# Performance work log

Measured on AMD Instinct MI355X. Metric: run time of the kernel, lower is better.

Reference implementation:

```python
import jax, jax.numpy as jnp
import numpy as np

N, T = 8, 64
V = [2048, 1024, 512, 256, 128]
E = [12288, 6144, 3072, 1536, 768]
NF = [1, 8, 16, 32, 64, 128]
LAT, INIT_DIM = 64, 16
K3 = 27  # 3x3x3 spline kernel bank


def setup_inputs():
    ks = iter(jax.random.split(jax.random.key(0), 80))
    inp = {}
    inp['x'] = jax.random.normal(next(ks), (N, V[0], T), jnp.float32)
    for l in range(5):
        inp['edge_index%d' % l] = jax.random.randint(next(ks), (2, E[l]), 0, V[l])
        inp['edge_attr%d' % l] = jax.random.uniform(next(ks), (E[l], 3), jnp.float32)
    pools = {'P01': (V[1], V[0]), 'P12': (V[2], V[1]), 'P23': (V[3], V[2]), 'P34': (V[4], V[3]),
             'P43': (V[3], V[4]), 'P32': (V[2], V[3]), 'P21': (V[1], V[2]), 'P10': (V[0], V[1])}
    for n, sh in pools.items():
        inp[n] = jax.random.normal(next(ks), sh, jnp.float32) / np.float32(np.sqrt(sh[1]))
    convs = {'conv1_w': (NF[0], NF[1]), 'conv2_w': (NF[1], NF[2]), 'conv3_w': (NF[2], NF[3]), 'conv4_w': (NF[3], NF[4]),
             'deconv4_w': (NF[4], NF[3]), 'deconv3_w': (NF[3], NF[2]), 'deconv2_w': (NF[2], NF[1]), 'deconv1_w': (NF[1], NF[0])}
    for n, (ci, co) in convs.items():
        inp[n] = jax.random.normal(next(ks), (K3, ci, co), jnp.float32) / np.float32(np.sqrt(ci * 8))
    def lin(k, o, i):
        return jax.random.normal(k, (o, i), jnp.float32) / np.float32(np.sqrt(i))
    inp['fce1_w'] = lin(next(ks), NF[5], NF[4]); inp['fce1_b'] = jnp.zeros((NF[5],), jnp.float32)
    inp['fce2_w'] = lin(next(ks), LAT, NF[5]); inp['fce2_b'] = jnp.zeros((LAT,), jnp.float32)
    inp['fcd3_w'] = lin(next(ks), NF[5], LAT); inp['fcd3_b'] = jnp.zeros((NF[5],), jnp.float32)
    inp['fcd4_w'] = lin(next(ks), NF[4], NF[5]); inp['fcd4_b'] = jnp.zeros((NF[4],), jnp.float32)
    for pre in ('dom', 'ini'):
        inp[pre + '_Wih'] = lin(next(ks), 3 * LAT, LAT)
        inp[pre + '_Whh'] = lin(next(ks), 3 * LAT, LAT)
        inp[pre + '_bih'] = jnp.zeros((3 * LAT,), jnp.float32)
        inp[pre + '_bhh'] = jnp.zeros((3 * LAT,), jnp.float32)
        inp[pre + '_agg_w'] = lin(next(ks), LAT, LAT)
        inp[pre + '_agg_b'] = jnp.zeros((LAT,), jnp.float32)
    for g in ('r', 'u', 'c'):
        inp['tr_W' + g] = lin(next(ks), LAT, 2 * LAT)
        inp['tr_b' + g] = jnp.zeros((LAT,), jnp.float32)
    return inp


def _edge_weights(attr, W):
    # Degree-1 B-spline basis over 3-dim pseudo-coords, kernel_size=3 per dim.
    pos = attr * 2.0                                    # [0, ks-1]
    i0 = jnp.clip(jnp.floor(pos), 0.0, 1.0).astype(jnp.int32)
    f = pos - i0                                        # fractional part
    We = jnp.zeros((attr.shape[0], W.shape[1], W.shape[2]), W.dtype)
    for c0 in (0, 1):
        w0 = f[:, 0] if c0 else 1.0 - f[:, 0]
        for c1 in (0, 1):
            w1 = f[:, 1] if c1 else 1.0 - f[:, 1]
            for c2 in (0, 1):
                w2 = f[:, 2] if c2 else 1.0 - f[:, 2]
                flat = (i0[:, 0] + c0) * 9 + (i0[:, 1] + c1) * 3 + (i0[:, 2] + c2)
                We = We + (w0 * w1 * w2)[:, None, None] * W[flat]
    return We                                           # (E, Ci, Co)


def _spatial_block(x, edge_index, edge_attr, W):
    # x: (N, V, Ci, T); edge-conditioned graph conv per time step, mean-aggregated, ELU.
    Nn, Vv, Ci, Tt = x.shape
    We = _edge_weights(edge_attr, W)                    # (E, Ci, Co)
    src, dst = edge_index[0], edge_index[1]
    msg = jnp.einsum('neit,eio->enot', x[:, src], We)   # (E, N, Co, T)
    agg = jax.ops.segment_sum(msg, dst, num_segments=Vv)
    deg = jax.ops.segment_sum(jnp.ones((dst.shape[0],), x.dtype), dst, num_segments=Vv)
    agg = agg / jnp.maximum(deg, 1.0)[:, None, None, None]
    return jax.nn.elu(agg.transpose(1, 0, 2, 3))        # (N, V, Co, T)


def _pw(x, Wl, b):
    # 1x1 Conv2d over channel dim: x (N, V, C, T)
    return jnp.einsum('nvct,oc->nvot', x, Wl) + b[None, None, :, None]


def _pool(h, P):
    # torch.matmul(P, x.view(N, V, C*T))
    Nn, Vv, Cc, Tt = h.shape
    return jnp.matmul(P, h.reshape(Nn, Vv, Cc * Tt)).reshape(Nn, P.shape[0], Cc, Tt)


def _rnn_encode(x, Wih, Whh, bih, bhh):
    # GRU over time per node; x (N, V, C, T) -> hidden seq (N, V, H, T)
    Nn, Vv, Cc, Tt = x.shape
    xt = x.transpose(3, 0, 1, 2).reshape(Tt, Nn * Vv, Cc)
    H = Whh.shape[1]
    def step(h, xi):
        gi = xi @ Wih.T + bih
        gh = h @ Whh.T + bhh
        ir, iz, ig = jnp.split(gi, 3, axis=-1)
        hr, hz, hg = jnp.split(gh, 3, axis=-1)
        r = jax.nn.sigmoid(ir + hr)
        z = jax.nn.sigmoid(iz + hz)
        g = jnp.tanh(ig + r * hg)
        hn = (1.0 - z) * g + z * h
        return hn, hn
    h0 = jnp.zeros((Nn * Vv, H), x.dtype)
    _, hs = jax.lax.scan(step, h0, xt)
    return hs.reshape(Tt, Nn, Vv, H).transpose(1, 2, 3, 0)


def reference(x, edge_attr0, edge_attr1, edge_attr2, edge_attr3, edge_attr4, P01, P12, P23, P34, P43, P32, P21, P10, conv1_w, conv2_w, conv3_w, conv4_w, deconv4_w, deconv3_w, deconv2_w, deconv1_w, fce1_w, fce1_b, fce2_w, fce2_b, fcd3_w, fcd3_b, fcd4_w, fcd4_b, dom_Wih, dom_Whh, dom_bih, dom_bhh, dom_agg_w, dom_agg_b, ini_Wih, ini_Whh, ini_bih, ini_bhh, ini_agg_w, ini_agg_b, tr_Wr, tr_br, tr_Wu, tr_bu, tr_Wc, tr_bc, edge_index0, edge_index1, edge_index2, edge_index3, edge_index4):
    h = x.reshape(N, V[0], NF[0], T)
    h = _pool(_spatial_block(h, edge_index0, edge_attr0, conv1_w), P01)
    h = _pool(_spatial_block(h, edge_index1, edge_attr1, conv2_w), P12)
    h = _pool(_spatial_block(h, edge_index2, edge_attr2, conv3_w), P23)
    h = _pool(_spatial_block(h, edge_index3, edge_attr3, conv4_w), P34)
    h = jax.nn.elu(_pw(h, fce1_w, fce1_b))
    embed = jnp.tanh(_pw(h, fce2_w, fce2_b))            # (N, V4, LAT, T)
    # ---- latent domain + initial state ----
    dom = _rnn_encode(embed, dom_Wih, dom_Whh, dom_bih, dom_bhh)
    z_D = jnp.tanh(dom[..., -1] @ dom_agg_w.T + dom_agg_b)
    ini = _rnn_encode(embed[..., :INIT_DIM], ini_Wih, ini_Whh, ini_bih, ini_bhh)
    z_0 = jnp.tanh(ini[..., -1] @ ini_agg_w.T + ini_agg_b)
    # ---- recurrent latent propagation over T steps (gated transition) ----
    def step(zp, _):
        cat = jnp.concatenate([zp, z_D], axis=-1)
        r = jax.nn.sigmoid(cat @ tr_Wr.T + tr_br)
        u = jax.nn.sigmoid(cat @ tr_Wu.T + tr_bu)
        c = jnp.tanh(jnp.concatenate([r * zp, z_D], axis=-1) @ tr_Wc.T + tr_bc)
        zt = (1.0 - u) * zp + u * c
        return zt, zt
    _, zs = jax.lax.scan(step, z_0, None, length=T)
    z = zs.transpose(1, 2, 3, 0)                        # (N, V4, LAT, T)
    h = jax.nn.elu(_pw(z, fcd3_w, fcd3_b))
    h = jax.nn.elu(_pw(h, fcd4_w, fcd4_b))
    h = _spatial_block(_pool(h, P43), edge_index3, edge_attr3, deconv4_w)
    h = _spatial_block(_pool(h, P32), edge_index2, edge_attr2, deconv3_w)
    h = _spatial_block(_pool(h, P21), edge_index1, edge_attr1, deconv2_w)
    h = _spatial_block(_pool(h, P10), edge_index0, edge_attr0, deconv1_w)
    return h.reshape(N, V[0], T)
```

## Files before the change

kernel.cpp:

```cpp
#include <hip/hip_runtime.h>

#define NB 8
#define TT 64

typedef __attribute__((ext_vector_type(8))) short bf16x8_t;
typedef __attribute__((ext_vector_type(4))) float f32x4_t;

__device__ __forceinline__ float sigm(float x){ return 1.0f/(1.0f+expf(-x)); }
__device__ __forceinline__ float eluf(float x){ return x>0.0f ? x : expm1f(x); }
__device__ __forceinline__ ushort f2bf(float f){
  uint u = __float_as_uint(f);
  return (ushort)((u + 0x7FFFu + ((u >> 16) & 1u)) >> 16);
}
__device__ __forceinline__ float bf2f(ushort u){
  return __uint_as_float(((uint)u) << 16);
}

__device__ __constant__ int c_VL[4] = {2048, 1024, 512, 256};
__device__ __constant__ int c_VO[4] = {0, 2048, 3072, 3584};
__device__ __constant__ int c_EO[4] = {0, 12288, 18432, 21504};
#define TOTV 3840
#define TOTE 23040

__global__ void transpose_kernel(const float* __restrict__ in, float* __restrict__ out, int R, int C){
// ... 86 lines not shown
  }
  if (tid == 0) rowptr_all[rbase + Vv] = s[2047];
}

__global__ void csr_fill(const int* __restrict__ d0, const int* __restrict__ d1,
                         const int* __restrict__ d2, const int* __restrict__ d3,
                         int* __restrict__ cursor_all, int* __restrict__ elist_all){
  int idx = blockIdx.x*256 + threadIdx.x;
  if (idx >= TOTE) return;
  int l = (idx < 12288) ? 0 : (idx < 18432) ? 1 : (idx < 21504) ? 2 : 3;
  int e = idx - c_EO[l];
  const int* dl = (l==0)?d0:(l==1)?d1:(l==2)?d2:d3;
  int p = atomicAdd(&cursor_all[c_VO[l] + dl[e]], 1);
  elist_all[p] = e;
}

__global__ void csr_sort(const int* __restrict__ rowptr_all, int* __restrict__ elist_all){
  int idx = blockIdx.x*256 + threadIdx.x;
  if (idx >= TOTV) return;
  int l = (idx < 2048) ? 0 : (idx < 3072) ? 1 : (idx < 3584) ? 2 : 3;
  int v = idx - c_VO[l];
  int rbase = c_VO[l] + l, eo = c_EO[l];
  int s = eo + rowptr_all[rbase + v], epos = eo + rowptr_all[rbase + v + 1];
  for (int i = s + 1; i < epos; ++i){
    int key = elist_all[i];
    int j = i - 1;
    while (j >= s && elist_all[j] > key){ elist_all[j+1] = elist_all[j]; --j; }
    elist_all[j+1] = key;
  }
}

__global__ void edge_we_kernel(const float* __restrict__ attr, const float* __restrict__ Wb,
                               float* __restrict__ We, int E, int CiCo){
  int idx = blockIdx.x*256 + threadIdx.x;
  if (idx >= E*CiCo) return;
  int e = idx / CiCo, r = idx - e*CiCo;
  float f[3]; int i0[3];
  #pragma unroll
  for (int d = 0; d < 3; ++d){
    float p  = attr[e*3+d]*2.0f;
    float fl = fminf(fmaxf(floorf(p), 0.0f), 1.0f);
    i0[d] = (int)fl;
    f[d]  = p - fl;
  }
  float acc = 0.0f;
  #pragma unroll
  for (int c0 = 0; c0 < 2; ++c0){
    float w0 = c0 ? f[0] : 1.0f - f[0];
    #pragma unroll
    for (int c1 = 0; c1 < 2; ++c1){
      float w1 = c1 ? f[1] : 1.0f - f[1];
      #pragma unroll
      for (int c2 = 0; c2 < 2; ++c2){
        float w2 = c2 ? f[2] : 1.0f - f[2];
        int flat = (i0[0]+c0)*9 + (i0[1]+c1)*3 + (i0[2]+c2);
        acc += w0*w1*w2 * Wb[flat*CiCo + r];
      }
    }
  }
  We[idx] = acc;
}

template<int Ci, int Co, int CiP>
__global__ __launch_bounds__(256) void edge_weT2(
    const float* __restrict__ attr, const float* __restrict__ Wb,
    ushort* __restrict__ WeT){
  __shared__ float s[Ci][Co + 1];
  int e = blockIdx.x, tid = threadIdx.x;
  float f[3]; int i0[3];
  #pragma unroll
  for (int d = 0; d < 3; ++d){
    float p  = attr[e*3+d]*2.0f;
    float fl = fminf(fmaxf(floorf(p), 0.0f), 1.0f);
    i0[d] = (int)fl;
    f[d]  = p - fl;
  }
  float w[8]; int fl8[8];
  #pragma unroll
  for (int c0 = 0; c0 < 2; ++c0)
    #pragma unroll
    for (int c1 = 0; c1 < 2; ++c1)
      #pragma unroll
      for (int c2 = 0; c2 < 2; ++c2){
        int k = c0*4 + c1*2 + c2;
        w[k] = (c0 ? f[0] : 1.0f - f[0]) * (c1 ? f[1] : 1.0f - f[1]) * (c2 ? f[2] : 1.0f - f[2]);
        fl8[k] = (i0[0]+c0)*9 + (i0[1]+c1)*3 + (i0[2]+c2);
      }
  constexpr int CiCo = Ci*Co;
  for (int r = tid; r < CiCo; r += 256){
    float acc = 0.0f;
    #pragma unroll
    for (int k = 0; k < 8; ++k) acc += w[k]*Wb[fl8[k]*CiCo + r];
    s[r/Co][r - (r/Co)*Co] = acc;
  }
  __syncthreads();
  ushort* op = WeT + (size_t)e*(Co*CiP);
  for (int r2 = tid; r2 < Co*CiP; r2 += 256){
    int co = r2 / CiP, ci = r2 - co*CiP;
    op[r2] = (ci < Ci) ? f2bf(s[ci][co]) : (ushort)0;
  }
}

template<int Ci, int Co>
__global__ __launch_bounds__(256) void gconv2_kernel(
    const float* __restrict__ x, const float* __restrict__ We,
    const int* __restrict__ src_arr, const int* __restrict__ rowptr,
    const int* __restrict__ elist, float* __restrict__ out, int V){
  constexpr int CiCo = Ci*Co;
  __shared__ float ws[4][CiCo];
  __shared__ float red[Co*64];
  int blk = blockIdx.x;
  int n = blk / V, v = blk - n*V;
  int tid = threadIdx.x;
  int w = tid >> 6, lane = tid & 63;
  int rs = rowptr[v], re = rowptr[v+1];
  float acc[Co];
  #pragma unroll
  for (int i = 0; i < Co; ++i) acc[i] = 0.0f;

  for (int q = rs + w; q < re; q += 4){
    int e   = elist[q];
    int src = src_arr[e];
    const float* wsrc = We + (size_t)e*CiCo;
    #pragma unroll
    for (int i = lane; i < CiCo; i += 64) ws[w][i] = wsrc[i];
    __builtin_amdgcn_s_waitcnt(0);
    const float* xp = x + ((size_t)(n*V + src))*(Ci*64) + lane;
    #pragma unroll 4
    for (int ci = 0; ci < Ci; ++ci){
      float xv = xp[(size_t)ci*64];
      if constexpr (Co >= 4){
        #pragma unroll
        for (int co = 0; co < Co; co += 4){
          float4 wv = *(const float4*)&ws[w][ci*Co + co];
          acc[co+0] += wv.x*xv;
          acc[co+1] += wv.y*xv;
          acc[co+2] += wv.z*xv;
          acc[co+3] += wv.w*xv;
        }
      } else {
        #pragma unroll
        for (int co = 0; co < Co; ++co) acc[co] += ws[w][ci*Co + co]*xv;
      }
    }
  }

  if (w == 0){
    #pragma unroll
    for (int co = 0; co < Co; ++co) red[co*64 + lane] = acc[co];
  }
  __syncthreads();
  #pragma unroll
  for (int ww = 1; ww < 4; ++ww){
    if (w == ww){
      #pragma unroll
      for (int co = 0; co < Co; ++co) red[co*64 + lane] += acc[co];
    }
    __syncthreads();
  }
  float scale = 1.0f / fmaxf((float)(re - rs), 1.0f);
  size_t ob = ((size_t)(n*V + v))*(Co*64);
  for (int co = w; co < Co; co += 4)
    out[ob + (size_t)co*64 + lane] = eluf(red[co*64 + lane]*scale);
}

template<int CiP, int Co>
__global__ __launch_bounds__(256, 4) void gconv_mfma4(
    const ushort* __restrict__ xT, const ushort* __restrict__ WeT,
    const int* __restrict__ src_arr, const int* __restrict__ rowptr,
    const int* __restrict__ elist, float* __restrict__ out, int V){
  constexpr int MT = Co/16, KT = CiP/32;
  __shared__ int2 es[64];
  __shared__ float red[Co*64];
  int blk = blockIdx.x;
  int n = blk / V, v = blk - n*V;
  int tid = threadIdx.x;
  int w = tid >> 6, lane = tid & 63;
  int l15 = lane & 15, g = lane >> 4;
  int rs = rowptr[v], re = rowptr[v+1];
  int deg = re - rs;
  int cnt0 = (deg < 64) ? deg : 64;
  if (tid < cnt0){
    int e = elist[rs + tid];
    es[tid] = make_int2(e, src_arr[e]);
  }
  __syncthreads();
  f32x4_t acc[MT][4];
  #pragma unroll
  for (int m = 0; m < MT; ++m)
    #pragma unroll
    for (int tt = 0; tt < 4; ++tt) acc[m][tt] = (f32x4_t){0.f,0.f,0.f,0.f};
  for (int q = w; q < deg; q += 4){
    int e, src;
    if (q < 64){ e = es[q].x; src = es[q].y; }
    else { e = elist[rs + q]; src = src_arr[e]; }
    const ushort* xp = xT + ((size_t)(n*V + src))*(64*CiP) + (size_t)l15*CiP + g*8;
    const ushort* wp = WeT + (size_t)e*(Co*CiP) + (size_t)l15*CiP + g*8;
    #pragma unroll
    for (int kt = 0; kt < KT; ++kt){
      bf16x8_t bfrag[4];
      #pragma unroll
      for (int tt = 0; tt < 4; ++tt)
        bfrag[tt] = *(const bf16x8_t*)(xp + (size_t)tt*16*CiP + kt*32);
      #pragma unroll
      for (int m = 0; m < MT; ++m){
        bf16x8_t afrag = *(const bf16x8_t*)(wp + (size_t)m*16*CiP + kt*32);
        #pragma unroll
        for (int tt = 0; tt < 4; ++tt)
          acc[m][tt] = __builtin_amdgcn_mfma_f32_16x16x32_bf16(afrag, bfrag[tt], acc[m][tt], 0, 0, 0);
      }
    }
  }
  if (w == 0){
    #pragma unroll
    for (int m = 0; m < MT; ++m)
      #pragma unroll
      for (int tt = 0; tt < 4; ++tt)
        #pragma unroll
        for (int r = 0; r < 4; ++r)
          red[(m*16 + g*4 + r)*64 + tt*16 + l15] = acc[m][tt][r];
  }
  __syncthreads();
  #pragma unroll
  for (int ww = 1; ww < 4; ++ww){
    if (w == ww){
      #pragma unroll
      for (int m = 0; m < MT; ++m)
        #pragma unroll
        for (int tt = 0; tt < 4; ++tt)
          #pragma unroll
          for (int r = 0; r < 4; ++r)
            red[(m*16 + g*4 + r)*64 + tt*16 + l15] += acc[m][tt][r];
    }
    __syncthreads();
  }
  float scale = 1.0f / fmaxf((float)deg, 1.0f);
  size_t ob = ((size_t)(n*V + v))*(Co*64);
  for (int i = tid; i < Co*64; i += 256)
    out[ob + i] = eluf(red[i]*scale);
}

template<int OUTBF>
__global__ __launch_bounds__(256) void pool_mfma64(
    const ushort* __restrict__ A, const ushort* __restrict__ BT, void* __restrict__ Cout,
    int M, int K, int NN){
  __shared__ ushort As[64*40];
  __shared__ ushort Bs[64*40];
  char* Asb = (char*)As; char* Bsb = (char*)Bs;
  int tid = threadIdx.x;
  int wv = tid >> 6, lane = tid & 63;
  int g = lane >> 4, l15 = lane & 15;
  int wr = wv >> 1, wc = wv & 1;
  int m0 = blockIdx.y*64, n0 = blockIdx.x*64;
  const ushort* Bp = BT + (size_t)blockIdx.z*((size_t)NN*K);
  f32x4_t acc[2][2];
  #pragma unroll
  for (int i = 0; i < 2; ++i)
    #pragma unroll
    for (int j = 0; j < 2; ++j) acc[i][j] = (f32x4_t){0.f,0.f,0.f,0.f};
  int srow = tid >> 2, slot = tid & 3;
  int wbo = srow*80 + slot*16;
  const ushort* gA = A  + (size_t)(m0+srow)*K + slot*8;
  const ushort* gB = Bp + (size_t)(n0+srow)*K + slot*8;
  for (int k0 = 0; k0 < K; k0 += 32){
    uint4 va = *(const uint4*)(gA + k0);
    uint4 vb = *(const uint4*)(gB + k0);
    __syncthreads();
    *(uint4*)(Asb + wbo) = va;
    *(uint4*)(Bsb + wbo) = vb;
    __syncthreads();
    bf16x8_t af[2], bfr[2];
    #pragma unroll
    for (int f = 0; f < 2; ++f){
      af[f]  = *(const bf16x8_t*)(Asb + (wr*32 + f*16 + l15)*80 + g*16);
      bfr[f] = *(const bf16x8_t*)(Bsb + (wc*32 + f*16 + l15)*80 + g*16);
    }
    #pragma unroll
    for (int fm = 0; fm < 2; ++fm)
      #pragma unroll
      for (int fn = 0; fn < 2; ++fn)
        acc[fm][fn] = __builtin_amdgcn_mfma_f32_16x16x32_bf16(af[fm], bfr[fn], acc[fm][fn], 0, 0, 0);
  }
  #pragma unroll
  for (int fm = 0; fm < 2; ++fm){
    int row = m0 + wr*32 + fm*16 + g*4;
    #pragma unroll
    for (int fn = 0; fn < 2; ++fn){
      int col = n0 + wc*32 + fn*16 + l15;
      if constexpr (OUTBF){
        ushort* Cb = (ushort*)Cout + (size_t)blockIdx.z*((size_t)M*NN);
        #pragma unroll
        for (int r = 0; r < 4; ++r)
          Cb[(size_t)(row + r)*NN + col] = f2bf(acc[fm][fn][r]);
      } else {
        float* Cf = (float*)Cout + (size_t)blockIdx.z*((size_t)M*NN);
        #pragma unroll
        for (int r = 0; r < 4; ++r)
          Cf[(size_t)(row + r)*NN + col] = acc[fm][fn][r];
      }
    }
  }
}

template<int C, int O, int ACT, int INF, int OUTF>
__global__ __launch_bounds__(256) void pw_mfma(
    const void* __restrict__ inv, const ushort* __restrict__ Wb, const float* __restrict__ bias,
    void* __restrict__ outv){
  constexpr int MT = O/16, KT = C/32;
  constexpr int CP = C + 8, OP = O + 8;
  __shared__ ushort XT[64*CP];
  __shared__ ushort YT[OUTF ? 64*OP : 64];
  int s = blockIdx.x, tid = threadIdx.x;
  int w = tid >> 6, lane = tid & 63;
  int l15 = lane & 15, g = lane >> 4;
  if constexpr (INF == 0){
    const float* ip = (const float*)inv + (size_t)s*C*64;
    for (int i = tid; i < C*64; i += 256){ int c = i >> 6, t = i & 63; XT[t*CP + c] = f2bf(ip[i]); }
  } else if constexpr (INF == 1){
    const float* ip = (const float*)inv + (size_t)s*64*C;
    for (int i = tid; i < C*64; i += 256){ int t = i / C, c = i - t*C; XT[t*CP + c] = f2bf(ip[i]); }
  } else {
    const ushort* ip = (const ushort*)inv + (size_t)s*64*C;
    for (int i = tid; i < C*64; i += 256){ int t = i / C, c = i - t*C; XT[t*CP + c] = ip[i]; }
  }
  __syncthreads();
  int trow = w*16 + l15;
  f32x4_t acc[MT];
  #pragma unroll
  for (int m = 0; m < MT; ++m) acc[m] = (f32x4_t){0.f,0.f,0.f,0.f};
  #pragma unroll
  for (int kt = 0; kt < KT; ++kt){
    bf16x8_t bfrag = *(const bf16x8_t*)(&XT[trow*CP + kt*32 + g*8]);
    #pragma unroll
    for (int m = 0; m < MT; ++m){
      bf16x8_t afrag = *(const bf16x8_t*)(Wb + (size_t)(m*16 + l15)*C + kt*32 + g*8);
      acc[m] = __builtin_amdgcn_mfma_f32_16x16x32_bf16(afrag, bfrag, acc[m], 0, 0, 0);
    }
  }
  if constexpr (OUTF == 0){
    float* op = (float*)outv + (size_t)s*O*64;
    #pragma unroll
    for (int m = 0; m < MT; ++m){
      #pragma unroll
      for (int r = 0; r < 4; ++r){
        int o = m*16 + g*4 + r;
        float v = acc[m][r] + bias[o];
        v = (ACT == 1) ? eluf(v) : tanhf(v);
        op[(size_t)o*64 + trow] = v;
      }
    }
  } else {
    #pragma unroll
    for (int m = 0; m < MT; ++m){
      #pragma unroll
      for (int r = 0; r < 4; ++r){
        int o = m*16 + g*4 + r;
        float v = acc[m][r] + bias[o];
        v = (ACT == 1) ? eluf(v) : tanhf(v);
        YT[trow*OP + o] = f2bf(v);
      }
    }
    __syncthreads();
    ushort* op = (ushort*)outv + (size_t)s*64*O;
    for (int i = tid; i < 64*O; i += 256){
      int t = i / O, o = i - t*O;
      op[i] = YT[t*OP + o];
    }
  }
}

template<int TSTEPS>
__global__ __launch_bounds__(192) void gru3_kernel(
    const ushort* __restrict__ GI,
    const float* __restrict__ WhhT,
    const float* __restrict__ bih, const float* __restrict__ bhh,
    const float* __restrict__ aggT, const float* __restrict__ aggb,
    float* __restrict__ zout){
  __shared__ float hsh[64];
  __shared__ float rbuf[64];
  __shared__ float zbuf[64];
  int s = blockIdx.x, tid = threadIdx.x;
  int g = tid >> 6, j = tid & 63;
  if (tid < 64) hsh[tid] = 0.0f;
  float whh[64];
  #pragma unroll
  for (int c = 0; c < 64; ++c) whh[c] = WhhT[c*192 + tid];
  float b_i = bih[tid], b_h = bhh[tid];
  const ushort* gp = GI + (size_t)s*64*256 + tid;
  float gi_cur = b_i + bf2f(gp[0]);
  __syncthreads();
  for (int t = 0; t < TSTEPS; ++t){
    ushort gnx = (t + 1 < TSTEPS) ? gp[(size_t)(t+1)*256] : (ushort)0;
    float gh0 = 0.f, gh1 = 0.f;
    #pragma unroll
    for (int c4 = 0; c4 < 16; ++c4){
      float4 hv = *(const float4*)&hsh[c4*4];
      gh0 += whh[c4*4+0]*hv.x; gh1 += whh[c4*4+1]*hv.y;
      gh0 += whh[c4*4+2]*hv.z; gh1 += whh[c4*4+3]*hv.w;
    }
    float gh = b_h + gh0 + gh1;
    if (g == 0)      rbuf[j] = sigm(gi_cur + gh);
    else if (g == 1) zbuf[j] = sigm(gi_cur + gh);
    __syncthreads();
    if (g == 2){
      float gg = tanhf(gi_cur + rbuf[j]*gh);
      float z  = zbuf[j];
      hsh[j] = (1.0f - z)*gg + z*hsh[j];
    }
    __syncthreads();
    gi_cur = b_i + bf2f(gnx);
  }
  if (tid < 64){
    float a = aggb[tid];
    #pragma unroll
    for (int c = 0; c < 64; ++c) a += aggT[c*64 + tid]*hsh[c];
    zout[(size_t)s*64 + tid] = tanhf(a);
  }
}

__global__ __launch_bounds__(192) void trans2_kernel(
    const float* __restrict__ z0, const float* __restrict__ zD,
    const float* __restrict__ WrT, const float* __restrict__ WuT, const float* __restrict__ WcT,
    const float* __restrict__ br, const float* __restrict__ bu, const float* __restrict__ bc,
    float* __restrict__ zs){
  __shared__ float zp[64];
  __shared__ float zd[64];
  __shared__ float rz[64];
  __shared__ float ubuf[64];
  int s = blockIdx.x, tid = threadIdx.x;
  int g = tid >> 6, j = tid & 63;
  if (tid < 64){ zp[tid] = z0[(size_t)s*64 + tid]; zd[tid] = zD[(size_t)s*64 + tid]; }
  const float* WT = (g == 0) ? WrT : (g == 1) ? WuT : WcT;
  const float* bb = (g == 0) ? br  : (g == 1) ? bu  : bc;
  float wv[64];
  #pragma unroll
  for (int c = 0; c < 64; ++c) wv[c] = WT[c*64 + j];
  float bconst = bb[j];
  __syncthreads();
  {
    float a0 = 0.f, a1 = 0.f;
    #pragma unroll
    for (int c4 = 0; c4 < 16; ++c4){
      float4 dv = *(const float4*)&zd[c4*4];
      a0 += WT[(64 + c4*4 + 0)*64 + j]*dv.x;
      a1 += WT[(64 + c4*4 + 1)*64 + j]*dv.y;
      a0 += WT[(64 + c4*4 + 2)*64 + j]*dv.z;
      a1 += WT[(64 + c4*4 + 3)*64 + j]*dv.w;
    }
    bconst += a0 + a1;
  }
  for (int t = 0; t < 64; ++t){
    if (g < 2){
      float a0 = 0.f, a1 = 0.f;
      #pragma unroll
      for (int c4 = 0; c4 < 16; ++c4){
        float4 pv = *(const float4*)&zp[c4*4];
        a0 += wv[c4*4+0]*pv.x; a1 += wv[c4*4+1]*pv.y;
        a0 += wv[c4*4+2]*pv.z; a1 += wv[c4*4+3]*pv.w;
      }
      float v = sigm(bconst + a0 + a1);
      if (g == 0) rz[j]   = v*zp[j];
      else        ubuf[j] = v;
    }
    __syncthreads();
    if (g == 2){
      float a0 = 0.f, a1 = 0.f;
      #pragma unroll
      for (int c4 = 0; c4 < 16; ++c4){
        float4 rv = *(const float4*)&rz[c4*4];
        a0 += wv[c4*4+0]*rv.x; a1 += wv[c4*4+1]*rv.y;
        a0 += wv[c4*4+2]*rv.z; a1 += wv[c4*4+3]*rv.w;
      }
      float cc = tanhf(bconst + a0 + a1);
      float u  = ubuf[j];
      float zt = (1.0f - u)*zp[j] + u*cc;
      zs[(size_t)s*4096 + t*64 + j] = zt;
      zp[j] = zt;
    }
    __syncthreads();
  }
}

extern "C" void kernel_launch(void* const* d_in, const int* in_sizes, int n_in,
                              void* d_out, int out_size, void* d_ws, size_t ws_size,
                              hipStream_t stream){
  static const int Vl[5] = {2048, 1024, 512, 256, 128};
  static const int El[5] = {12288, 6144, 3072, 1536, 768};
  static const int VO[4] = {0, 2048, 3072, 3584};
  static const int EO[4] = {0, 12288, 18432, 21504};

  const float* xin = (const float*)d_in[0];
  const int*   ei[4]; const float* ea[4];
  for (int l = 0; l < 4; ++l){ ei[l] = (const int*)d_in[1 + 2*l]; ea[l] = (const float*)d_in[2 + 2*l]; }
  const float* Psrc[8] = {(const float*)d_in[11], (const float*)d_in[12], (const float*)d_in[13], (const float*)d_in[14],
                          (const float*)d_in[15], (const float*)d_in[16], (const float*)d_in[17], (const float*)d_in[18]};
  const float* conv_w[4]   = {(const float*)d_in[19], (const float*)d_in[20], (const float*)d_in[21], (const float*)d_in[22]};
  const float* deconv_w[4] = {(const float*)d_in[23], (const float*)d_in[24], (const float*)d_in[25], (const float*)d_in[26]};
  const float* fce1_w = (const float*)d_in[27]; const float* fce1_b = (const float*)d_in[28];
  const float* fce2_w = (const float*)d_in[29]; const float* fce2_b = (const float*)d_in[30];
  const float* fcd3_w = (const float*)d_in[31]; const float* fcd3_b = (const float*)d_in[32];
  const float* fcd4_w = (const float*)d_in[33]; const float* fcd4_b = (const float*)d_in[34];
  const float* dom_Wih = (const float*)d_in[35]; const float* dom_Whh = (const float*)d_in[36];
  const float* dom_bih = (const float*)d_in[37]; const float* dom_bhh = (const float*)d_in[38];
  const float* dom_aggw = (const float*)d_in[39]; const float* dom_aggb = (const float*)d_in[40];
  const float* ini_Wih = (const float*)d_in[41]; const float* ini_Whh = (const float*)d_in[42];
  const float* ini_bih = (const float*)d_in[43]; const float* ini_bhh = (const float*)d_in[44];
  const float* ini_aggw = (const float*)d_in[45]; const float* ini_aggb = (const float*)d_in[46];
  const float* tr_Wr = (const float*)d_in[47]; const float* tr_br = (const float*)d_in[48];
  const float* tr_Wu = (const float*)d_in[49]; const float* tr_bu = (const float*)d_in[50];
  const float* tr_Wc = (const float*)d_in[51]; const float* tr_bc = (const float*)d_in[52];

  char* wsp = (char*)d_ws;
  size_t off = 0;
  auto carve = [&](size_t bytes) -> void* {
    void* p = wsp + off;
    off = (off + bytes + 255) & ~(size_t)255;
    return p;
  };
  const size_t BUFCAP = (size_t)NB*2048*8*64;
  float* bufA = (float*)carve(BUFCAP*4);
  float* bufB = (float*)carve(BUFCAP*4);
  void* webt = carve((size_t)NB*1024*1024*2 + 1024);
  float*  We = (float*)webt;
  ushort* BT = (ushort*)webt;
  ushort* xT = (ushort*)webt;
  ushort* h1B = (ushort*)webt;
  ushort* WeTb = (ushort*)carve((size_t)1536*64*32*2 + 1024);
  ushort* embB2 = (ushort*)carve((size_t)1024*64*64*2);
  float* zD   = (float*)carve((size_t)NB*128*64*4);
  float* z0   = (float*)carve((size_t)NB*128*64*4);
  float* domWhhT = (float*)carve(12288*4);
  float* iniWhhT = (float*)carve(12288*4);
  float* domAggT = (float*)carve(4096*4);
  float* iniAggT = (float*)carve(4096*4);
  float* trWrT   = (float*)carve(8192*4);
  float* trWuT   = (float*)carve(8192*4);
  float* trWcT   = (float*)carve(8192*4);
  ushort* WihPadD = (ushort*)carve(256*64*2);
  ushort* WihPadI = (ushort*)carve(256*64*2);
  ushort* Wfce1b = (ushort*)carve(8192*2);
  ushort* Wfce2b = (ushort*)carve(8192*2);
  ushort* Wfcd3b = (ushort*)carve(8192*2);
  ushort* Wfcd4b = (ushort*)carve(8192*2);
  static const int PM[8] = {1024, 512, 256, 128, 256, 512, 1024, 2048};
  static const int PK[8] = {2048, 1024, 512, 256, 128, 256, 512, 1024};
  ushort* Pb[8];
  for (int i = 0; i < 8; ++i) Pb[i] = (ushort*)carve((size_t)PM[i]*PK[i]*2);
  int* deg_all    = (int*)carve(TOTV*4);
  int* cursor_all = (int*)carve(TOTV*4);
  int* rowptr_all = (int*)carve((TOTV + 4)*4);
  int* elist_all  = (int*)carve(TOTE*4);
  (void)ws_size; (void)in_sizes; (void)n_in; (void)out_size;

  auto tr = [&](const float* in, float* out, int R, int C){
    transpose_kernel<<<(R*C + 255)/256, 256, 0, stream>>>(in, out, R, C);
  };
  tr(dom_Whh, domWhhT, 192, 64);  tr(ini_Whh, iniWhhT, 192, 64);
  tr(dom_aggw, domAggT, 64, 64);  tr(ini_aggw, iniAggT, 64, 64);
  tr(tr_Wr, trWrT, 64, 128);  tr(tr_Wu, trWuT, 64, 128);  tr(tr_Wc, trWcT, 64, 128);
  pad_wih<<<64, 256, 0, stream>>>(dom_Wih, WihPadD);
  pad_wih<<<64, 256, 0, stream>>>(ini_Wih, WihPadI);
  conv_bf16<<<32, 256, 0, stream>>>(fce1_w, Wfce1b, 8192);
  conv_bf16<<<32, 256, 0, stream>>>(fce2_w, Wfce2b, 8192);
  conv_bf16<<<32, 256, 0, stream>>>(fcd3_w, Wfcd3b, 8192);
  conv_bf16<<<32, 256, 0, stream>>>(fcd4_w, Wfcd4b, 8192);
  for (int i = 0; i < 8; ++i){
    int nel = PM[i]*PK[i];
    conv_bf16<<<(nel + 255)/256, 256, 0, stream>>>(Psrc[i], Pb[i], nel);
  }

  const int* dsts[4] = {ei[0] + El[0], ei[1] + El[1], ei[2] + El[2], ei[3] + El[3]};
  csr_zero<<<(TOTV + 255)/256, 256, 0, stream>>>(deg_all);
  csr_deg <<<(TOTE + 255)/256, 256, 0, stream>>>(dsts[0], dsts[1], dsts[2], dsts[3], deg_all);
  csr_scan<<<4, 1024, 0, stream>>>(deg_all, rowptr_all, cursor_all);
  csr_fill<<<(TOTE + 255)/256, 256, 0, stream>>>(dsts[0], dsts[1], dsts[2], dsts[3], cursor_all, elist_all);
  csr_sort<<<(TOTV + 255)/256, 256, 0, stream>>>(rowptr_all, elist_all);

  auto gconv = [&](const float* in, float* out, int l, const float* Wb, int Ci, int Co){
    int CiCo = Ci*Co;
    int tot = El[l]*CiCo;
    edge_we_kernel<<<(tot + 255)/256, 256, 0, stream>>>(ea[l], Wb, We, El[l], CiCo);
    int nblk = NB*Vl[l];
    const int* rp = rowptr_all + VO[l] + l;
    const int* el = elist_all + EO[l];
    #define GCASE(CI,CO) if (Ci==CI && Co==CO) gconv2_kernel<CI,CO><<<nblk, 256, 0, stream>>>(in, We, ei[l], rp, el, out, Vl[l]);
    GCASE(1,8)  GCASE(8,16)  GCASE(16,8)  GCASE(8,1)
    #undef GCASE
  };
  auto gconv_m = [&](const float* in, float* out, int l, const float* Wb, int Ci, int Co){
    int S = NB*Vl[l];
    int CiP = (Ci < 32) ? 32 : Ci;
    if (Ci == 16)      xpose_bf16<16,32><<<S, 256, 0, stream>>>(in, xT);
    else if (Ci == 32) xpose_bf16<32,32><<<S, 256, 0, stream>>>(in, xT);
    else               xpose_bf16<64,64><<<S, 256, 0, stream>>>(in, xT);
    if (Ci == 16 && Co == 32)      edge_weT2<16,32,32><<<El[l], 256, 0, stream>>>(ea[l], Wb, WeTb);
    else if (Ci == 32 && Co == 64) edge_weT2<32,64,32><<<El[l], 256, 0, stream>>>(ea[l], Wb, WeTb);
    else if (Ci == 64 && Co == 32) edge_weT2<64,32,64><<<El[l], 256, 0, stream>>>(ea[l], Wb, WeTb);
    else if (Ci == 32 && Co == 16) edge_weT2<32,16,32><<<El[l], 256, 0, stream>>>(ea[l], Wb, WeTb);
    const int* rp = rowptr_all + VO[l] + l;
    const int* el = elist_all + EO[l];
    #define GMC(CIP,CO) if (CiP==CIP && Co==CO) gconv_mfma4<CIP,CO><<<S, 256, 0, stream>>>(xT, WeTb, ei[l], rp, el, out, Vl[l]);
    GMC(32,32) GMC(32,64) GMC(64,32) GMC(32,16)
    #undef GMC
  };
  auto pool2 = [&](int pi, const float* hin, float* out, int M, int K, int NN){
    dim3 tg(NN/64, K/64, NB);
    transp_bf16<<<tg, 256, 0, stream>>>(hin, BT, K, NN);
    dim3 g(NN/64, M/64, NB);
    pool_mfma64<0><<<g, 256, 0, stream>>>(Pb[pi], BT, (void*)out, M, K, NN);
  };

  gconv(xin,  bufA, 0, conv_w[0], 1, 8);
  pool2(0, bufA, bufB, 1024, 2048, 512);
  gconv(bufB, bufA, 1, conv_w[1], 8, 16);
  pool2(1, bufA, bufB, 512, 1024, 1024);
  gconv_m(bufB, bufA, 2, conv_w[2], 16, 32);
  pool2(2, bufA, bufB, 256, 512, 2048);
  gconv_m(bufB, bufA, 3, conv_w[3], 32, 64);
  pool2(3, bufA, bufB, 128, 256, 4096);

  pw_mfma<64,128,1,0,1><<<1024, 256, 0, stream>>>(bufB, Wfce1b, fce1_b, h1B);
  pw_mfma<128,64,2,2,1><<<1024, 256, 0, stream>>>(h1B, Wfce2b, fce2_b, embB2);

  dim3 gg(4, 1024, 1);
  pool_mfma64<1><<<gg, 256, 0, stream>>>(embB2, WihPadD, (void*)bufA, 65536, 64, 256);
  gru3_kernel<64><<<NB*128, 192, 0, stream>>>((const ushort*)bufA, domWhhT, dom_bih, dom_bhh, domAggT, dom_aggb, zD);
  pool_mfma64<1><<<gg, 256, 0, stream>>>(embB2, WihPadI, (void*)bufA, 65536, 64, 256);
  gru3_kernel<16><<<NB*128, 192, 0, stream>>>((const ushort*)bufA, iniWhhT, ini_bih, ini_bhh, iniAggT, ini_aggb, z0);
  trans2_kernel<<<NB*128, 192, 0, stream>>>(z0, zD, trWrT, trWuT, trWcT, tr_br, tr_bu, tr_bc, bufA);

  pw_mfma<64,128,1,1,1><<<1024, 256, 0, stream>>>(bufA, Wfcd3b, fcd3_b, h1B);
  pw_mfma<128,64,1,2,0><<<1024, 256, 0, stream>>>(h1B, Wfcd4b, fcd4_b, bufA);
  pool2(4, bufA, bufB, 256, 128, 4096);
  gconv_m(bufB, bufA, 3, deconv_w[0], 64, 32);
  pool2(5, bufA, bufB, 512, 256, 2048);
  gconv_m(bufB, bufA, 2, deconv_w[1], 32, 16);
  pool2(6, bufA, bufB, 1024, 512, 1024);
  gconv(bufB, bufA, 1, deconv_w[2], 16, 8);
  pool2(7, bufA, bufB, 2048, 1024, 512);
  gconv(bufB, (float*)d_out, 0, deconv_w[3], 8, 1);
}
```

Measured before the change: 835.9 us.

## Collapse GRU and transition kernels to single-wavefront blocks with per-thread gates

The recurrent GRU and gated-transition kernels drop from 192-thread blocks, where each 64-thread group computed one gate, to 64-thread blocks where each thread holds all three gate weight columns in registers. Gate exchanges now stay in registers instead of going through shared buffers, so work-group barriers cost less and idle gate groups go away. The price is about 192 weight registers per thread, which lowers occupancy, and three times the serial FMA work per thread on each timestep.

```diff
diff --git a/kernel.cpp b/kernel.cpp
--- a/kernel.cpp
+++ b/kernel.cpp
@@ -480,113 +480,122 @@
 }
 
 template<int TSTEPS>
-__global__ __launch_bounds__(192) void gru3_kernel(
+__global__ __launch_bounds__(64) void gru4_kernel(
     const ushort* __restrict__ GI,
     const float* __restrict__ WhhT,
     const float* __restrict__ bih, const float* __restrict__ bhh,
     const float* __restrict__ aggT, const float* __restrict__ aggb,
     float* __restrict__ zout){
-  __shared__ float hsh[64];
-  __shared__ float rbuf[64];
-  __shared__ float zbuf[64];
-  int s = blockIdx.x, tid = threadIdx.x;
-  int g = tid >> 6, j = tid & 63;
-  if (tid < 64) hsh[tid] = 0.0f;
-  float whh[64];
-  #pragma unroll
-  for (int c = 0; c < 64; ++c) whh[c] = WhhT[c*192 + tid];
-  float b_i = bih[tid], b_h = bhh[tid];
-  const ushort* gp = GI + (size_t)s*64*256 + tid;
-  float gi_cur = b_i + bf2f(gp[0]);
+  __shared__ float hs[64];
+  int s = blockIdx.x, j = threadIdx.x;
+  float wr[64], wz[64], wg[64];
+  #pragma unroll
+  for (int c = 0; c < 64; ++c){
+    wr[c] = WhhT[c*192 + j];
+    wz[c] = WhhT[c*192 + 64 + j];
+    wg[c] = WhhT[c*192 + 128 + j];
+  }
+  float bir = bih[j], biz = bih[64+j], big = bih[128+j];
+  float bhr = bhh[j], bhz = bhh[64+j], bhg = bhh[128+j];
+  float h_j = 0.0f;
+  hs[j] = 0.0f;
+  const ushort* gp = GI + (size_t)s*64*256;
+  ushort cr = gp[j], cz = gp[64+j], cg = gp[128+j];
   __syncthreads();
   for (int t = 0; t < TSTEPS; ++t){
-    ushort gnx = (t + 1 < TSTEPS) ? gp[(size_t)(t+1)*256] : (ushort)0;
-    float gh0 = 0.f, gh1 = 0.f;
+    ushort nr = 0, nz = 0, ng = 0;
+    if (t + 1 < TSTEPS){
+      nr = gp[(size_t)(t+1)*256 + j];
+      nz = gp[(size_t)(t+1)*256 + 64 + j];
+      ng = gp[(size_t)(t+1)*256 + 128 + j];
+    }
+    float hr0=0.f, hr1=0.f, hz0=0.f, hz1=0.f, hg0=0.f, hg1=0.f;
     #pragma unroll
     for (int c4 = 0; c4 < 16; ++c4){
-      float4 hv = *(const float4*)&hsh[c4*4];
-      gh0 += whh[c4*4+0]*hv.x; gh1 += whh[c4*4+1]*hv.y;
-      gh0 += whh[c4*4+2]*hv.z; gh1 += whh[c4*4+3]*hv.w;
-    }
-    float gh = b_h + gh0 + gh1;
-    if (g == 0)      rbuf[j] = sigm(gi_cur + gh);
-    else if (g == 1) zbuf[j] = sigm(gi_cur + gh);
-    __syncthreads();
-    if (g == 2){
-      float gg = tanhf(gi_cur + rbuf[j]*gh);
-      float z  = zbuf[j];
-      hsh[j] = (1.0f - z)*gg + z*hsh[j];
-    }
-    __syncthreads();
-    gi_cur = b_i + bf2f(gnx);
-  }
-  if (tid < 64){
-    float a = aggb[tid];
-    #pragma unroll
-    for (int c = 0; c < 64; ++c) a += aggT[c*64 + tid]*hsh[c];
-    zout[(size_t)s*64 + tid] = tanhf(a);
-  }
-}
-
-__global__ __launch_bounds__(192) void trans2_kernel(
+      float4 hv = *(const float4*)&hs[c4*4];
+      hr0 += wr[c4*4+0]*hv.x; hr1 += wr[c4*4+1]*hv.y;
+      hr0 += wr[c4*4+2]*hv.z; hr1 += wr[c4*4+3]*hv.w;
+      hz0 += wz[c4*4+0]*hv.x; hz1 += wz[c4*4+1]*hv.y;
+      hz0 += wz[c4*4+2]*hv.z; hz1 += wz[c4*4+3]*hv.w;
+      hg0 += wg[c4*4+0]*hv.x; hg1 += wg[c4*4+1]*hv.y;
+      hg0 += wg[c4*4+2]*hv.z; hg1 += wg[c4*4+3]*hv.w;
+    }
+    float r = sigm(bir + bf2f(cr) + bhr + hr0 + hr1);
+    float z = sigm(biz + bf2f(cz) + bhz + hz0 + hz1);
+    float g = tanhf(big + bf2f(cg) + r*(bhg + hg0 + hg1));
+    h_j = (1.0f - z)*g + z*h_j;
+    __syncthreads();
+    hs[j] = h_j;
+    __syncthreads();
+    cr = nr; cz = nz; cg = ng;
+  }
+  float a = aggb[j];
+  #pragma unroll
+  for (int c = 0; c < 64; ++c) a += aggT[c*64 + j]*hs[c];
+  zout[(size_t)s*64 + j] = tanhf(a);
+}
+
+__global__ __launch_bounds__(64) void trans3_kernel(
     const float* __restrict__ z0, const float* __restrict__ zD,
     const float* __restrict__ WrT, const float* __restrict__ WuT, const float* __restrict__ WcT,
     const float* __restrict__ br, const float* __restrict__ bu, const float* __restrict__ bc,
     float* __restrict__ zs){
-  __shared__ float zp[64];
-  __shared__ float zd[64];
-  __shared__ float rz[64];
-  __shared__ float ubuf[64];
-  int s = blockIdx.x, tid = threadIdx.x;
-  int g = tid >> 6, j = tid & 63;
-  if (tid < 64){ zp[tid] = z0[(size_t)s*64 + tid]; zd[tid] = zD[(size_t)s*64 + tid]; }
-  const float* WT = (g == 0) ? WrT : (g == 1) ? WuT : WcT;
-  const float* bb = (g == 0) ? br  : (g == 1) ? bu  : bc;
-  float wv[64];
-  #pragma unroll
-  for (int c = 0; c < 64; ++c) wv[c] = WT[c*64 + j];
-  float bconst = bb[j];
+  __shared__ float zps[64];
+  __shared__ float zds[64];
+  __shared__ float rzs[64];
+  int s = blockIdx.x, j = threadIdx.x;
+  float zp_j = z0[(size_t)s*64 + j];
+  zps[j] = zp_j;
+  zds[j] = zD[(size_t)s*64 + j];
+  float wr[64], wu[64], wc[64];
+  #pragma unroll
+  for (int c = 0; c < 64; ++c){
+    wr[c] = WrT[c*64 + j];
+    wu[c] = WuT[c*64 + j];
+    wc[c] = WcT[c*64 + j];
+  }
+  float bcr = br[j], bcu = bu[j], bcc = bc[j];
   __syncthreads();
   {
-    float a0 = 0.f, a1 = 0.f;
+    float r0=0.f,r1=0.f,u0=0.f,u1=0.f,c0=0.f,c1=0.f;
     #pragma unroll
     for (int c4 = 0; c4 < 16; ++c4){
-      float4 dv = *(const float4*)&zd[c4*4];
-      a0 += WT[(64 + c4*4 + 0)*64 + j]*dv.x;
-      a1 += WT[(64 + c4*4 + 1)*64 + j]*dv.y;
-      a0 += WT[(64 + c4*4 + 2)*64 + j]*dv.z;
-      a1 += WT[(64 + c4*4 + 3)*64 + j]*dv.w;
-    }
-    bconst += a0 + a1;
+      float4 dv = *(const float4*)&zds[c4*4];
+      r0 += WrT[(64+c4*4+0)*64+j]*dv.x; r1 += WrT[(64+c4*4+1)*64+j]*dv.y;
+      r0 += WrT[(64+c4*4+2)*64+j]*dv.z; r1 += WrT[(64+c4*4+3)*64+j]*dv.w;
+      u0 += WuT[(64+c4*4+0)*64+j]*dv.x; u1 += WuT[(64+c4*4+1)*64+j]*dv.y;
+      u0 += WuT[(64+c4*4+2)*64+j]*dv.z; u1 += WuT[(64+c4*4+3)*64+j]*dv.w;
+      c0 += WcT[(64+c4*4+0)*64+j]*dv.x; c1 += WcT[(64+c4*4+1)*64+j]*dv.y;
+      c0 += WcT[(64+c4*4+2)*64+j]*dv.z; c1 += WcT[(64+c4*4+3)*64+j]*dv.w;
+    }
+    bcr += r0 + r1; bcu += u0 + u1; bcc += c0 + c1;
   }
   for (int t = 0; t < 64; ++t){
-    if (g < 2){
-      float a0 = 0.f, a1 = 0.f;
-      #pragma unroll
-      for (int c4 = 0; c4 < 16; ++c4){
-        float4 pv = *(const float4*)&zp[c4*4];
-        a0 += wv[c4*4+0]*pv.x; a1 += wv[c4*4+1]*pv.y;
-        a0 += wv[c4*4+2]*pv.z; a1 += wv[c4*4+3]*pv.w;
-      }
-      float v = sigm(bconst + a0 + a1);
-      if (g == 0) rz[j]   = v*zp[j];
-      else        ubuf[j] = v;
-    }
-    __syncthreads();
-    if (g == 2){
-      float a0 = 0.f, a1 = 0.f;
-      #pragma unroll
-      for (int c4 = 0; c4 < 16; ++c4){
-        float4 rv = *(const float4*)&rz[c4*4];
-        a0 += wv[c4*4+0]*rv.x; a1 += wv[c4*4+1]*rv.y;
-        a0 += wv[c4*4+2]*rv.z; a1 += wv[c4*4+3]*rv.w;
-      }
-      float cc = tanhf(bconst + a0 + a1);
-      float u  = ubuf[j];
-      float zt = (1.0f - u)*zp[j] + u*cc;
-      zs[(size_t)s*4096 + t*64 + j] = zt;
-      zp[j] = zt;
-    }
+    float ar0=0.f, ar1=0.f, au0=0.f, au1=0.f;
+    #pragma unroll
+    for (int c4 = 0; c4 < 16; ++c4){
+      float4 pv = *(const float4*)&zps[c4*4];
+      ar0 += wr[c4*4+0]*pv.x; ar1 += wr[c4*4+1]*pv.y;
+      ar0 += wr[c4*4+2]*pv.z; ar1 += wr[c4*4+3]*pv.w;
+      au0 += wu[c4*4+0]*pv.x; au1 += wu[c4*4+1]*pv.y;
+      au0 += wu[c4*4+2]*pv.z; au1 += wu[c4*4+3]*pv.w;
+    }
+    float r = sigm(bcr + ar0 + ar1);
+    float u = sigm(bcu + au0 + au1);
+    rzs[j] = r*zp_j;
+    __syncthreads();
+    float ac0=0.f, ac1=0.f;
+    #pragma unroll
+    for (int c4 = 0; c4 < 16; ++c4){
+      float4 rv = *(const float4*)&rzs[c4*4];
+      ac0 += wc[c4*4+0]*rv.x; ac1 += wc[c4*4+1]*rv.y;
+      ac0 += wc[c4*4+2]*rv.z; ac1 += wc[c4*4+3]*rv.w;
+    }
+    float cc = tanhf(bcc + ac0 + ac1);
+    float zt = (1.0f - u)*zp_j + u*cc;
+    zs[(size_t)s*4096 + t*64 + j] = zt;
+    zp_j = zt;
+    zps[j] = zt;
     __syncthreads();
   }
 }
@@ -734,10 +743,10 @@
 
   dim3 gg(4, 1024, 1);
   pool_mfma64<1><<<gg, 256, 0, stream>>>(embB2, WihPadD, (void*)bufA, 65536, 64, 256);
-  gru3_kernel<64><<<NB*128, 192, 0, stream>>>((const ushort*)bufA, domWhhT, dom_bih, dom_bhh, domAggT, dom_aggb, zD);
+  gru4_kernel<64><<<NB*128, 64, 0, stream>>>((const ushort*)bufA, domWhhT, dom_bih, dom_bhh, domAggT, dom_aggb, zD);
   pool_mfma64<1><<<gg, 256, 0, stream>>>(embB2, WihPadI, (void*)bufA, 65536, 64, 256);
-  gru3_kernel<16><<<NB*128, 192, 0, stream>>>((const ushort*)bufA, iniWhhT, ini_bih, ini_bhh, iniAggT, ini_aggb, z0);
-  trans2_kernel<<<NB*128, 192, 0, stream>>>(z0, zD, trWrT, trWuT, trWcT, tr_br, tr_bu, tr_bc, bufA);
+  gru4_kernel<16><<<NB*128, 64, 0, stream>>>((const ushort*)bufA, iniWhhT, ini_bih, ini_bhh, iniAggT, ini_aggb, z0);
+  trans3_kernel<<<NB*128, 64, 0, stream>>>(z0, zD, trWrT, trWuT, trWcT, tr_br, tr_bu, tr_bc, bufA);
 
   pw_mfma<64,128,1,1,1><<<1024, 256, 0, stream>>>(bufA, Wfcd3b, fcd3_b, h1B);
   pw_mfma<128,64,1,2,0><<<1024, 256, 0, stream>>>(h1B, Wfcd4b, fcd4_b, bufA);
```

After: 853.8 us. +2.2%, slower.

## Fuse paired pointwise MFMA layers and merge both GRU encoders into one launch

Applied to the files above, without the earlier changes.

Each pair of 1x1 pointwise layers (fce1+fce2, fcd3+fcd4) now runs in one kernel that keeps the 128-channel intermediate in LDS as bf16, so it no longer round-trips through global memory. The domain and initial GRU encoders run in a single launch with twice the blocks, after both input-projection GEMMs write to separate buffers. This removes kernel launches and intermediate traffic and lets the short 16-step GRU blocks overlap with the 64-step ones. In exchange the fused kernel uses more LDS per block, and the merged GRU has runtime step counts and pointer selects instead of template constants.

```diff
diff --git a/kernel.cpp b/kernel.cpp
--- a/kernel.cpp
+++ b/kernel.cpp
@@ -412,84 +412,124 @@
   }
 }
 
-template<int C, int O, int ACT, int INF, int OUTF>
-__global__ __launch_bounds__(256) void pw_mfma(
-    const void* __restrict__ inv, const ushort* __restrict__ Wb, const float* __restrict__ bias,
+template<int C, int O1, int O2, int ACT1, int ACT2, int INF, int OUTF>
+__global__ __launch_bounds__(256) void pw2_mfma(
+    const void* __restrict__ inv,
+    const ushort* __restrict__ W1, const float* __restrict__ b1,
+    const ushort* __restrict__ W2, const float* __restrict__ b2,
     void* __restrict__ outv){
-  constexpr int MT = O/16, KT = C/32;
-  constexpr int CP = C + 8, OP = O + 8;
+  constexpr int CP = C + 8, O1P = O1 + 8;
+  constexpr int MT1 = O1/16, KT1 = C/32;
+  constexpr int MT2 = O2/16, KT2 = O1/32;
   __shared__ ushort XT[64*CP];
-  __shared__ ushort YT[OUTF ? 64*OP : 64];
+  __shared__ ushort YT[64*O1P];
   int s = blockIdx.x, tid = threadIdx.x;
   int w = tid >> 6, lane = tid & 63;
   int l15 = lane & 15, g = lane >> 4;
   if constexpr (INF == 0){
     const float* ip = (const float*)inv + (size_t)s*C*64;
     for (int i = tid; i < C*64; i += 256){ int c = i >> 6, t = i & 63; XT[t*CP + c] = f2bf(ip[i]); }
-  } else if constexpr (INF == 1){
+  } else {
     const float* ip = (const float*)inv + (size_t)s*64*C;
     for (int i = tid; i < C*64; i += 256){ int t = i / C, c = i - t*C; XT[t*CP + c] = f2bf(ip[i]); }
-  } else {
-    const ushort* ip = (const ushort*)inv + (size_t)s*64*C;
-    for (int i = tid; i < C*64; i += 256){ int t = i / C, c = i - t*C; XT[t*CP + c] = ip[i]; }
   }
   __syncthreads();
   int trow = w*16 + l15;
-  f32x4_t acc[MT];
-  #pragma unroll
-  for (int m = 0; m < MT; ++m) acc[m] = (f32x4_t){0.f,0.f,0.f,0.f};
-  #pragma unroll
-  for (int kt = 0; kt < KT; ++kt){
-    bf16x8_t bfrag = *(const bf16x8_t*)(&XT[trow*CP + kt*32 + g*8]);
-    #pragma unroll
-    for (int m = 0; m < MT; ++m){
-      bf16x8_t afrag = *(const bf16x8_t*)(Wb + (size_t)(m*16 + l15)*C + kt*32 + g*8);
-      acc[m] = __builtin_amdgcn_mfma_f32_16x16x32_bf16(afrag, bfrag, acc[m], 0, 0, 0);
-    }
-  }
-  if constexpr (OUTF == 0){
-    float* op = (float*)outv + (size_t)s*O*64;
-    #pragma unroll
-    for (int m = 0; m < MT; ++m){
+  {
+    f32x4_t acc[MT1];
+    #pragma unroll
+    for (int m = 0; m < MT1; ++m) acc[m] = (f32x4_t){0.f,0.f,0.f,0.f};
+    #pragma unroll
+    for (int kt = 0; kt < KT1; ++kt){
+      bf16x8_t bfrag = *(const bf16x8_t*)(&XT[trow*CP + kt*32 + g*8]);
+      #pragma unroll
+      for (int m = 0; m < MT1; ++m){
+        bf16x8_t afrag = *(const bf16x8_t*)(W1 + (size_t)(m*16 + l15)*C + kt*32 + g*8);
+        acc[m] = __builtin_amdgcn_mfma_f32_16x16x32_bf16(afrag, bfrag, acc[m], 0, 0, 0);
+      }
+    }
+    #pragma unroll
+    for (int m = 0; m < MT1; ++m){
       #pragma unroll
       for (int r = 0; r < 4; ++r){
         int o = m*16 + g*4 + r;
-        float v = acc[m][r] + bias[o];
-        v = (ACT == 1) ? eluf(v) : tanhf(v);
-        op[(size_t)o*64 + trow] = v;
-      }
-    }
-  } else {
-    #pragma unroll
-    for (int m = 0; m < MT; ++m){
-      #pragma unroll
-      for (int r = 0; r < 4; ++r){
-        int o = m*16 + g*4 + r;
-        float v = acc[m][r] + bias[o];
-        v = (ACT == 1) ? eluf(v) : tanhf(v);
-        YT[trow*OP + o] = f2bf(v);
-      }
-    }
-    __syncthreads();
-    ushort* op = (ushort*)outv + (size_t)s*64*O;
-    for (int i = tid; i < 64*O; i += 256){
-      int t = i / O, o = i - t*O;
-      op[i] = YT[t*OP + o];
-    }
-  }
-}
-
-template<int TSTEPS>
-__global__ __launch_bounds__(192) void gru3_kernel(
-    const ushort* __restrict__ GI,
-    const float* __restrict__ WhhT,
-    const float* __restrict__ bih, const float* __restrict__ bhh,
-    const float* __restrict__ aggT, const float* __restrict__ aggb,
-    float* __restrict__ zout){
+        float v = acc[m][r] + b1[o];
+        v = (ACT1 == 1) ? eluf(v) : tanhf(v);
+        YT[trow*O1P + o] = f2bf(v);
+      }
+    }
+  }
+  __syncthreads();
+  {
+    f32x4_t acc[MT2];
+    #pragma unroll
+    for (int m = 0; m < MT2; ++m) acc[m] = (f32x4_t){0.f,0.f,0.f,0.f};
+    #pragma unroll
+    for (int kt = 0; kt < KT2; ++kt){
+      bf16x8_t bfrag = *(const bf16x8_t*)(&YT[trow*O1P + kt*32 + g*8]);
+      #pragma unroll
+      for (int m = 0; m < MT2; ++m){
+        bf16x8_t afrag = *(const bf16x8_t*)(W2 + (size_t)(m*16 + l15)*O1 + kt*32 + g*8);
+        acc[m] = __builtin_amdgcn_mfma_f32_16x16x32_bf16(afrag, bfrag, acc[m], 0, 0, 0);
+      }
+    }
+    if constexpr (OUTF == 0){
+      float* op = (float*)outv + (size_t)s*O2*64;
+      #pragma unroll
+      for (int m = 0; m < MT2; ++m){
+        #pragma unroll
+        for (int r = 0; r < 4; ++r){
+          int o = m*16 + g*4 + r;
+          float v = acc[m][r] + b2[o];
+          v = (ACT2 == 1) ? eluf(v) : tanhf(v);
+          op[(size_t)o*64 + trow] = v;
+        }
+      }
+    } else {
+      constexpr int O2P = O2 + 8;
+      #pragma unroll
+      for (int m = 0; m < MT2; ++m){
+        #pragma unroll
+        for (int r = 0; r < 4; ++r){
+          int o = m*16 + g*4 + r;
+          float v = acc[m][r] + b2[o];
+          v = (ACT2 == 1) ? eluf(v) : tanhf(v);
+          XT[trow*O2P + o] = f2bf(v);
+        }
+      }
+      __syncthreads();
+      ushort* op = (ushort*)outv + (size_t)s*64*O2;
+      for (int i = tid; i < 64*O2; i += 256){
+        int t = i / O2, o = i - t*O2;
+        op[i] = XT[t*O2P + o];
+      }
+    }
+  }
+}
+
+__global__ __launch_bounds__(192) void gru3m_kernel(
+    const ushort* __restrict__ GI_d, const ushort* __restrict__ GI_i,
+    const float* __restrict__ WhhT_d, const float* __restrict__ WhhT_i,
+    const float* __restrict__ bih_d, const float* __restrict__ bhh_d,
+    const float* __restrict__ aggT_d, const float* __restrict__ aggb_d,
+    const float* __restrict__ bih_i, const float* __restrict__ bhh_i,
+    const float* __restrict__ aggT_i, const float* __restrict__ aggb_i,
+    float* __restrict__ zD, float* __restrict__ z0, int S){
   __shared__ float hsh[64];
   __shared__ float rbuf[64];
   __shared__ float zbuf[64];
-  int s = blockIdx.x, tid = threadIdx.x;
+  int bid = blockIdx.x;
+  bool dom = (bid < S);
+  int s = dom ? bid : bid - S;
+  int TS = dom ? 64 : 16;
+  const ushort* GI   = dom ? GI_d   : GI_i;
+  const float* WhhT  = dom ? WhhT_d : WhhT_i;
+  const float* bih   = dom ? bih_d  : bih_i;
+  const float* bhh   = dom ? bhh_d  : bhh_i;
+  const float* aggT  = dom ? aggT_d : aggT_i;
+  const float* aggb  = dom ? aggb_d : aggb_i;
+  float* zout        = dom ? zD     : z0;
+  int tid = threadIdx.x;
   int g = tid >> 6, j = tid & 63;
   if (tid < 64) hsh[tid] = 0.0f;
   float whh[64];
@@ -499,8 +539,8 @@
   const ushort* gp = GI + (size_t)s*64*256 + tid;
   float gi_cur = b_i + bf2f(gp[0]);
   __syncthreads();
-  for (int t = 0; t < TSTEPS; ++t){
-    ushort gnx = (t + 1 < TSTEPS) ? gp[(size_t)(t+1)*256] : (ushort)0;
+  for (int t = 0; t < TS; ++t){
+    ushort gnx = (t + 1 < TS) ? gp[(size_t)(t+1)*256] : (ushort)0;
     float gh0 = 0.f, gh1 = 0.f;
     #pragma unroll
     for (int c4 = 0; c4 < 16; ++c4){
@@ -634,7 +674,6 @@
   float*  We = (float*)webt;
   ushort* BT = (ushort*)webt;
   ushort* xT = (ushort*)webt;
-  ushort* h1B = (ushort*)webt;
   ushort* WeTb = (ushort*)carve((size_t)1536*64*32*2 + 1024);
   ushort* embB2 = (ushort*)carve((size_t)1024*64*64*2);
   float* zD   = (float*)carve((size_t)NB*128*64*4);
@@ -729,24 +768,23 @@
   gconv_m(bufB, bufA, 3, conv_w[3], 32, 64);
   pool2(3, bufA, bufB, 128, 256, 4096);
 
-  pw_mfma<64,128,1,0,1><<<1024, 256, 0, stream>>>(bufB, Wfce1b, fce1_b, h1B);
-  pw_mfma<128,64,2,2,1><<<1024, 256, 0, stream>>>(h1B, Wfce2b, fce2_b, embB2);
+  pw2_mfma<64,128,64,1,2,0,1><<<1024, 256, 0, stream>>>(bufB, Wfce1b, fce1_b, Wfce2b, fce2_b, embB2);
 
   dim3 gg(4, 1024, 1);
   pool_mfma64<1><<<gg, 256, 0, stream>>>(embB2, WihPadD, (void*)bufA, 65536, 64, 256);
-  gru3_kernel<64><<<NB*128, 192, 0, stream>>>((const ushort*)bufA, domWhhT, dom_bih, dom_bhh, domAggT, dom_aggb, zD);
-  pool_mfma64<1><<<gg, 256, 0, stream>>>(embB2, WihPadI, (void*)bufA, 65536, 64, 256);
-  gru3_kernel<16><<<NB*128, 192, 0, stream>>>((const ushort*)bufA, iniWhhT, ini_bih, ini_bhh, iniAggT, ini_aggb, z0);
+  pool_mfma64<1><<<gg, 256, 0, stream>>>(embB2, WihPadI, (void*)bufB, 65536, 64, 256);
+  gru3m_kernel<<<2*NB*128, 192, 0, stream>>>((const ushort*)bufA, (const ushort*)bufB,
+      domWhhT, iniWhhT, dom_bih, dom_bhh, domAggT, dom_aggb,
+      ini_bih, ini_bhh, iniAggT, ini_aggb, zD, z0, NB*128);
   trans2_kernel<<<NB*128, 192, 0, stream>>>(z0, zD, trWrT, trWuT, trWcT, tr_br, tr_bu, tr_bc, bufA);
 
-  pw_mfma<64,128,1,1,1><<<1024, 256, 0, stream>>>(bufA, Wfcd3b, fcd3_b, h1B);
-  pw_mfma<128,64,1,2,0><<<1024, 256, 0, stream>>>(h1B, Wfcd4b, fcd4_b, bufA);
-  pool2(4, bufA, bufB, 256, 128, 4096);
-  gconv_m(bufB, bufA, 3, deconv_w[0], 64, 32);
-  pool2(5, bufA, bufB, 512, 256, 2048);
-  gconv_m(bufB, bufA, 2, deconv_w[1], 32, 16);
-  pool2(6, bufA, bufB, 1024, 512, 1024);
-  gconv(bufB, bufA, 1, deconv_w[2], 16, 8);
-  pool2(7, bufA, bufB, 2048, 1024, 512);
-  gconv(bufB, (float*)d_out, 0, deconv_w[3], 8, 1);
-}
+  pw2_mfma<64,128,64,1,1,1,0><<<1024, 256, 0, stream>>>(bufA, Wfcd3b, fcd3_b, Wfcd4b, fcd4_b, bufB);
+  pool2(4, bufB, bufA, 256, 128, 4096);
+  gconv_m(bufA, bufB, 3, deconv_w[0], 64, 32);
+  pool2(5, bufB, bufA, 512, 256, 2048);
+  gconv_m(bufA, bufB, 2, deconv_w[1], 32, 16);
+  pool2(6, bufB, bufA, 1024, 512, 1024);
+  gconv(bufA, bufB, 1, deconv_w[2], 16, 8);
+  pool2(7, bufB, bufA, 2048, 1024, 512);
+  gconv(bufA, (float*)d_out, 0, deconv_w[3], 8, 1);
+}
```

Measured after the change: 808.9 us. -3.2%, faster.
